# Kernel tuning notes

Hardware: AMD Instinct MI355X
Metric: run time of the kernel (lower is better)

The kernel has to match this reference:

```python
import jax, jax.numpy as jnp
import numpy as np

B, NWORD, HID = 4, 24, 512


def setup_inputs() -> dict:
    key = jax.random.key(0)
    ks = jax.random.split(key, 7)
    H = HID
    scale_in = 1.0 / np.sqrt(H)
    return {
        "seqt": jax.random.normal(ks[0], (B, NWORD, 2 * H), dtype=jnp.float32),
        # ins_input_linearity: Linear(H -> 5H) with bias
        "Wi": jax.random.normal(ks[1], (5 * H, H), dtype=jnp.float32) * scale_in,
        "bi": jnp.zeros((5 * H,), dtype=jnp.float32),
        # ins_state_linearity: Linear(H -> 5H) with bias (bias init: forget slots = 1)
        "Ws": jax.random.normal(ks[2], (5 * H, H), dtype=jnp.float32) * scale_in,
        "bs": jnp.zeros((5 * H,), dtype=jnp.float32).at[H:2 * H].set(1.0),
        # ins_bilinearity: BilinearSimilarity(2H, 2H) -> scalar x^T W y
        "Wbil": jax.random.normal(ks[3], (2 * H, 2 * H), dtype=jnp.float32) * (1.0 / (2.0 * H)),
    }


def reference(seqt, Wi, bi, Ws, bs, Wbil):
    """Inside pass (do_inside) of DioLstm in training mode (soft_sum over splits).

    Chart cell (left, L) covers words [left, left+L]. Returns root v = concat(h, c).
    """
    Bn, n, twoH = seqt.shape
    H = twoH // 2
    # ins_bias buffer: ones on the two forget-gate slots [H:3H]
    ins_bias = jnp.zeros((5 * H,), dtype=seqt.dtype).at[H:3 * H].set(1.0)

    def single(seq):  # seq: [n, 2H]
        chartH = jnp.zeros((n, n, H), seq.dtype).at[:, 0].set(seq[:, :H])
        chartC = jnp.zeros((n, n, H), seq.dtype).at[:, 0].set(seq[:, H:])
        chartS = jnp.zeros((n, n), seq.dtype)  # leaf scores are 0
        for L in range(1, n):  # span length - 1 (static unroll over diagonals)
            P = n - L  # number of spans on this diagonal
            lefts = jnp.arange(P)[:, None]          # [P,1]
            ksplit = jnp.arange(L)[None, :]          # [1,L]
            # left child: (left, k); right child: (left+k+1, L-1-k)
            lH = chartH[lefts, ksplit]; lC = chartC[lefts, ksplit]; lS = chartS[lefts, ksplit]
            ridx = lefts + ksplit + 1
            rlen = jnp.broadcast_to(L - 1 - ksplit, ridx.shape)
            rH = chartH[ridx, rlen]; rC = chartC[ridx, rlen]; rS = chartS[ridx, rlen]
            lv = jnp.concatenate([lH, lC], axis=-1)  # [P,L,2H]
            rv = jnp.concatenate([rH, rC], axis=-1)
            # bilinear compatibility + child scores
            compat = jnp.einsum('pki,ij,pkj->pk', lv, Wbil, rv) + lS + rS  # [P,L]
            # projected_input + projected_state (sum once; gate slices of the sum)
            proj = (lH @ Wi.T + bi + ins_bias) + (rH @ Ws.T + bs)  # [P,L,5H]
            ig, lf, rf, g, og = jnp.split(proj, 5, axis=-1)
            ig = jax.nn.sigmoid(ig); lf = jax.nn.sigmoid(lf); rf = jax.nn.sigmoid(rf)
            g = jnp.tanh(g); og = jax.nn.sigmoid(og)
            mem = lf * lC + rf * rC + ig * g
            h = og * jnp.tanh(mem)  # [P,L,H]
            # soft_sum: torch.tensor(s_set) detaches scores -> stop_gradient on weights
            sw = jax.lax.stop_gradient(compat)
            w = jax.nn.softmax(sw, axis=-1)  # [P,L]
            Hnew = jnp.einsum('pk,pkh->ph', w, h)
            Cnew = jnp.einsum('pk,pkh->ph', w, mem)
            Snew = jnp.sum(w * sw, axis=-1)
            pidx = jnp.arange(P)
            chartH = chartH.at[pidx, L].set(Hnew)
            chartC = chartC.at[pidx, L].set(Cnew)
            chartS = chartS.at[pidx, L].set(Snew)
        # root cell v = concat(h, c)
        return jnp.concatenate([chartH[0, n - 1], chartC[0, n - 1]], axis=0)

    return jax.vmap(single)(seqt)  # [B, 2H]
```

## Files before the change

### kernel.cpp

```cpp
#include <hip/hip_runtime.h>
#include <math.h>

#define NB 4
#define NW 24
#define H 512
#define H2 1024
#define H5 2560
#define NCELL 300
#define NEED_BYTES ((size_t)72<<20)

static float* g_buf = nullptr;
__attribute__((constructor)) static void dio_alloc_ws(){
  (void)hipMalloc((void**)&g_buf, NEED_BYTES);
}

typedef __attribute__((ext_vector_type(8))) short bf16x8;
typedef __attribute__((ext_vector_type(4))) float f32x4;
typedef unsigned short ushort_t;

__device__ __forceinline__ int coff(int l){ return l*NW - (l*(l-1))/2; }
__device__ __forceinline__ float sigm(float x){ return 1.f/(1.f+__expf(-x)); }
__device__ __forceinline__ float ftanh(float x){ return 1.f - 2.f/(__expf(2.f*x)+1.f); }

__device__ __forceinline__ ushort_t f2b(float x){
  unsigned int u = __float_as_uint(x);
  u += 0x7FFF + ((u>>16)&1);
  return (ushort_t)(u>>16);
}
__device__ __forceinline__ float b2f(ushort_t h){
  return __uint_as_float(((unsigned int)h)<<16);
}
__device__ __forceinline__ void split_store(ushort_t* __restrict__ ph,
                                            ushort_t* __restrict__ pl,
                                            size_t idx, float x){
  ushort_t h = f2b(x);
  ph[idx] = h;
  pl[idx] = f2b(x - b2f(h));
}

__device__ __forceinline__ float compat_dot(const float* __restrict__ cU,
                                            const float* __restrict__ cH,
                                            const float* __restrict__ cC,
                                            const float* __restrict__ cS,
                                            int lc, int rc, int lane){
  const float4* U4  = (const float4*)(cU + (size_t)lc*H2);
  const float4* Hr4 = (const float4*)(cH + (size_t)rc*H);
  const float4* Cr4 = (const float4*)(cC + (size_t)rc*H);
  float p = 0.f;
  #pragma unroll
  for (int it=0; it<2; it++){
    float4 u = U4[lane + 64*it], h = Hr4[lane + 64*it];
    p += u.x*h.x + u.y*h.y + u.z*h.z + u.w*h.w;
  }
  #pragma unroll
  for (int it=0; it<2; it++){
    float4 u = U4[128 + lane + 64*it], c = Cr4[lane + 64*it];
    p += u.x*c.x + u.y*c.y + u.z*c.z + u.w*c.w;
  }
  #pragma unroll
  for (int off=32; off>0; off>>=1) p += __shfl_down(p, off);
  return p + cS[lc] + cS[rc];
}

__global__ void k_init(const float* __restrict__ seqt,
                       const float* __restrict__ Wi, const float* __restrict__ Ws,
                       const float* __restrict__ Wbil,
                       ushort_t* __restrict__ WiBh, ushort_t* __restrict__ WiBl,
                       ushort_t* __restrict__ WsBh, ushort_t* __restrict__ WsBl,
                       ushort_t* __restrict__ WbilTh, ushort_t* __restrict__ WbilTl,
                       float* __restrict__ cH, float* __restrict__ cC, float* __restrict__ cS,
                       ushort_t* __restrict__ cHbh, ushort_t* __restrict__ cHbl,
                       ushort_t* __restrict__ cCbh, ushort_t* __restrict__ cCbl){
  const int blk = blockIdx.x, t = threadIdx.x;
  if (blk < 10240){
    int i = blk*256 + t;
    const int n = H5*H;
    if (i < n) split_store(WiBh, WiBl, i, Wi[i]);
    else       split_store(WsBh, WsBl, i-n, Ws[i-n]);
  } else if (blk < 11264){
    __shared__ float tile[32][33];
    int tb = blk - 10240;
    int tr = (tb>>5)*32, tc = (tb&31)*32;
    int tx = t & 31, ty = t >> 5;
    #pragma unroll
    for (int i=0;i<32;i+=8)
      tile[ty+i][tx] = Wbil[(size_t)(tr+ty+i)*H2 + tc+tx];
    __syncthreads();
    #pragma unroll
    for (int i=0;i<32;i+=8)
      split_store(WbilTh, WbilTl, (size_t)(tc+ty+i)*H2 + tr+tx, tile[tx][ty+i]);
  } else {
    int tid = (blk-11264)*256 + t;
    if (tid < NB*NW*H){
      int b = tid/(NW*H); int r = tid%(NW*H); int i = r/H; int d = r%H;
      size_t idx = (size_t)(b*NCELL + i)*H + d;
      float hv = seqt[(size_t)(b*NW+i)*H2 + d];
      float cv = seqt[(size_t)(b*NW+i)*H2 + H + d];
      cH[idx]=hv; cC[idx]=cv;
      split_store(cHbh,cHbl,idx,hv);
      split_store(cCbh,cCbl,idx,cv);
      if (d==0) cS[b*NCELL+i] = 0.f;
    }
  }
}

__device__ __forceinline__ void mfma3(f32x4& acc, bf16x8 ah, bf16x8 al,
                                      bf16x8 bh, bf16x8 bl){
  acc = __builtin_amdgcn_mfma_f32_16x16x32_bf16(ah, bh, acc, 0,0,0);
  acc = __builtin_amdgcn_mfma_f32_16x16x32_bf16(ah, bl, acc, 0,0,0);
  acc = __builtin_amdgcn_mfma_f32_16x16x32_bf16(al, bh, acc, 0,0,0);
}

__global__ void __launch_bounds__(512)
k_projN(const ushort_t* __restrict__ WiBh, const ushort_t* __restrict__ WiBl,
        const ushort_t* __restrict__ WsBh, const ushort_t* __restrict__ WsBl,
        const ushort_t* __restrict__ WbilTh, const ushort_t* __restrict__ WbilTl,
        const float* __restrict__ bi, const float* __restrict__ bs,
        const ushort_t* __restrict__ cHbh, const ushort_t* __restrict__ cHbl,
        const ushort_t* __restrict__ cCbh, const ushort_t* __restrict__ cCbl,
        float* __restrict__ cPI, float* __restrict__ cPS, float* __restrict__ cU,
        int d, int P)
{
  __shared__ f32x4 red[8][64];
  const int t = threadIdx.x, wave = t>>6, lane = t&63;
  const int jt = blockIdx.x;
  const int m0 = blockIdx.y*16;
  const int Mtot = NB*P;
  const int nm = min(16, Mtot-m0);

  int kind, j0;
  if (jt < 160){ kind=0; j0 = jt*16; }
  else if (jt < 320){ kind=1; j0 = (jt-160)*16; }
  else { kind=2; j0 = (jt-320)*16; }

  const int r = lane & 15;
  const int q = lane >> 4;

  int mg = m0 + (r < nm ? r : 0);
  const size_t arow = (size_t)((mg/P)*NCELL + coff(d) + mg%P)*H;

  f32x4 acc = {0.f,0.f,0.f,0.f};

  if (kind < 2){
    const ushort_t* bh_ = (kind==0 ? WiBh : WsBh) + (size_t)(j0+r)*H;
    const ushort_t* bl_ = (kind==0 ? WiBl : WsBl) + (size_t)(j0+r)*H;
    const int ks = wave*64 + q*8;
    bf16x8 fah[2], fal[2], fbh[2], fbl[2];
    #pragma unroll
    for (int s=0;s<2;s++){
      const int ko = ks + s*32;
      fah[s] = *(const bf16x8*)(cHbh + arow + ko);
      fal[s] = *(const bf16x8*)(cHbl + arow + ko);
      fbh[s] = *(const bf16x8*)(bh_ + ko);
      fbl[s] = *(const bf16x8*)(bl_ + ko);
    }
    #pragma unroll
    for (int s=0;s<2;s++) mfma3(acc, fah[s], fal[s], fbh[s], fbl[s]);
  } else {
    const ushort_t* bh_ = WbilTh + (size_t)(j0+r)*H2;
    const ushort_t* bl_ = WbilTl + (size_t)(j0+r)*H2;
    const ushort_t* ah_ = (wave<4 ? cHbh : cCbh) + arow;
    const ushort_t* al_ = (wave<4 ? cHbl : cCbl) + arow;
    const int kg0 = wave*128;
    const int ka0 = kg0 & 511;
    bf16x8 fah[4], fal[4], fbh[4], fbl[4];
    #pragma unroll
    for (int s=0;s<4;s++){
      const int so = s*32 + q*8;
      fah[s] = *(const bf16x8*)(ah_ + ka0 + so);
      fal[s] = *(const bf16x8*)(al_ + ka0 + so);
      fbh[s] = *(const bf16x8*)(bh_ + kg0 + so);
      fbl[s] = *(const bf16x8*)(bl_ + kg0 + so);
    }
    #pragma unroll
    for (int s=0;s<4;s++) mfma3(acc, fah[s], fal[s], fbh[s], fbl[s]);
  }

  red[wave][lane] = acc;
  __syncthreads();
  if (wave == 0){
    f32x4 s0=red[0][lane], s1=red[1][lane], s2=red[2][lane], s3=red[3][lane];
    f32x4 s4=red[4][lane], s5=red[5][lane], s6=red[6][lane], s7=red[7][lane];
    f32x4 tot = ((s0+s1)+(s2+s3)) + ((s4+s5)+(s6+s7));
    const int jo = j0 + r;
    float bias = 0.f;
    if (kind==0) bias = bi[jo] + ((jo>=H && jo<3*H)?1.f:0.f);
    else if (kind==1) bias = bs[jo];
    #pragma unroll
    for (int reg=0; reg<4; reg++){
      const int m = q*4 + reg;
      if (m < nm){
        const int mg2 = m0 + m;
        const size_t cell = (size_t)((mg2/P)*NCELL + coff(d) + mg2%P);
        const float v = tot[reg];
        if (kind==0)      cPI[cell*H5 + jo] = v + bias;
        else if (kind==1) cPS[cell*H5 + jo] = v + bias;
        else              cU [cell*H2 + jo] = v;
      }
    }
  }
}

__global__ void __launch_bounds__(256)
k_combine3(const float* __restrict__ cPI, const float* __restrict__ cPS,
           const float* __restrict__ cU,
           float* __restrict__ cH, float* __restrict__ cC, float* __restrict__ cS,
           ushort_t* __restrict__ cHbh, ushort_t* __restrict__ cHbl,
           ushort_t* __restrict__ cCbh, ushort_t* __restrict__ cCbl,
           const float* __restrict__ compatR, float* __restrict__ compatW,
           int L, int P){
  const int t = threadIdx.x;
  const int lane = t & 63;
  const int wave = t >> 6;
  const int nphase = NB*P*16;
  const int blk = blockIdx.x;

  if (blk >= nphase){
    const int P1 = P-1;
    const int nterm = L-1;
    int tid = (blk-nphase)*4 + wave;
    if (P1 > 0 && nterm > 0 && tid < NB*P1*nterm){
      int cell1 = tid / nterm;
      int k = 1 + tid % nterm;
      int b = cell1 / P1, left = cell1 % P1;
      int lc = b*NCELL + coff(k) + left;
      int rc = b*NCELL + coff(L-k) + left+k+1;
      float v = compat_dot(cU, cH, cC, cS, lc, rc, lane);
      if (lane==0) compatW[(b*NW + left)*NW + k] = v;
    }
    return;
  }

  const int cellid = blk >> 4;
  const int dg = blk & 15;
  const int b = cellid / P;
  const int left = cellid % P;
  __shared__ float compat_s[32];
  __shared__ float wts_s[32];
  __shared__ float S_s;
  __shared__ float partH[8][32];
  __shared__ float partC[8][32];

  if (wave == 0){
    int lc = b*NCELL + left;
    int rc = b*NCELL + coff(L-1) + left+1;
    float v = compat_dot(cU, cH, cC, cS, lc, rc, lane);
    if (lane==0) compat_s[0] = v;
  } else if (wave == 1 && L >= 2){
    int lc = b*NCELL + coff(L-1) + left;
    int rc = b*NCELL + left+L;
    float v = compat_dot(cU, cH, cC, cS, lc, rc, lane);
    if (lane==0) compat_s[L-1] = v;
  }
  if (t >= 1 && t <= L-2) compat_s[t] = compatR[(b*NW + left)*NW + t];
  __syncthreads();
  if (t==0){
    float mx = -1e30f;
    for (int k=0;k<L;k++) mx = fmaxf(mx, compat_s[k]);
    float den = 0.f;
    for (int k=0;k<L;k++){ float e = __expf(compat_s[k]-mx); wts_s[k]=e; den+=e; }
    float inv = 1.f/den, S = 0.f;
    for (int k=0;k<L;k++){ wts_s[k]*=inv; S += wts_s[k]*compat_s[k]; }
    S_s = S;
  }
  __syncthreads();
  const int dloc = t & 31;
  const int dim = dg*32 + dloc;
  const int kpar = t >> 5;
  float aH = 0.f, aC = 0.f;
  for (int k=kpar; k<L; k+=8){
    float wk = wts_s[k];
    int lc = b*NCELL + coff(k) + left;
    int rc = b*NCELL + coff(L-1-k) + left+k+1;
    const float* PI = cPI + (size_t)lc*H5;
    const float* PS = cPS + (size_t)rc*H5;
    float p0 = PI[dim]     + PS[dim];
    float p1 = PI[H+dim]   + PS[H+dim];
    float p2 = PI[2*H+dim] + PS[2*H+dim];
    float p3 = PI[3*H+dim] + PS[3*H+dim];
    float p4 = PI[4*H+dim] + PS[4*H+dim];
    float lcv = cC[(size_t)lc*H + dim];
    float rcv = cC[(size_t)rc*H + dim];
    float mem = sigm(p1)*lcv + sigm(p2)*rcv + sigm(p0)*ftanh(p3);
    float h = sigm(p4)*ftanh(mem);
    aH += wk*h; aC += wk*mem;
  }
  if (kpar > 0){ partH[kpar][dloc]=aH; partC[kpar][dloc]=aC; }
  __syncthreads();
  if (kpar == 0){
    #pragma unroll
    for (int q=1;q<8;q++){ aH += partH[q][dloc]; aC += partC[q][dloc]; }
    size_t nc = (size_t)(b*NCELL + coff(L) + left);
    cH[nc*H + dim] = aH;
    cC[nc*H + dim] = aC;
    split_store(cHbh,cHbl, nc*H + dim, aH);
    split_store(cCbh,cCbl, nc*H + dim, aC);
    if (t==0 && dg==0) cS[nc] = S_s;
  }
}

__global__ void k_out(const float* __restrict__ cH, const float* __restrict__ cC,
                      float* __restrict__ out){
  int tid = blockIdx.x*256+threadIdx.x;
  if (tid >= NB*H2) return;
  int b = tid>>10, d = tid&1023;
  int cell = b*NCELL + 299;
  out[tid] = (d<H) ? cH[(size_t)cell*H + d] : cC[(size_t)cell*H + (d-H)];
}

extern "C" void kernel_launch(void* const* d_in, const int* in_sizes, int n_in,
                              void* d_out, int out_size, void* d_ws, size_t ws_size,
                              hipStream_t stream){
  const float* seqt = (const float*)d_in[0];
  const float* Wi   = (const float*)d_in[1];
  const float* bi   = (const float*)d_in[2];
  const float* Ws   = (const float*)d_in[3];
  const float* bs   = (const float*)d_in[4];
  const float* Wbil = (const float*)d_in[5];
  float* out = (float*)d_out;

  float* p = (ws_size >= NEED_BYTES && g_buf == nullptr) ? (float*)d_ws : g_buf;
  float* cH  = p; p += (size_t)NB*NCELL*H;
  float* cC  = p; p += (size_t)NB*NCELL*H;
  float* cS  = p; p += (size_t)NB*NCELL;
  float* cPI = p; p += (size_t)NB*NCELL*H5;
  float* cPS = p; p += (size_t)NB*NCELL*H5;
  float* cU  = p; p += (size_t)NB*NCELL*H2;
  float* compatA = p; p += (size_t)NB*NW*NW;
  float* compatB = p; p += (size_t)NB*NW*NW;
  ushort_t* u = (ushort_t*)p;
  ushort_t* WiBh   = u; u += (size_t)H5*H;
  ushort_t* WiBl   = u; u += (size_t)H5*H;
  ushort_t* WsBh   = u; u += (size_t)H5*H;
  ushort_t* WsBl   = u; u += (size_t)H5*H;
  ushort_t* WbilTh = u; u += (size_t)H2*H2;
  ushort_t* WbilTl = u; u += (size_t)H2*H2;
  ushort_t* cHbh   = u; u += (size_t)NB*NCELL*H;
  ushort_t* cHbl   = u; u += (size_t)NB*NCELL*H;
  ushort_t* cCbh   = u; u += (size_t)NB*NCELL*H;
  ushort_t* cCbl   = u; u += (size_t)NB*NCELL*H;

  k_init<<<11456, 256, 0, stream>>>(seqt, Wi, Ws, Wbil,
      WiBh, WiBl, WsBh, WsBl, WbilTh, WbilTl,
      cH, cC, cS, cHbh, cHbl, cCbh, cCbl);

  k_projN<<<dim3(384, (NB*NW+15)/16), 512, 0, stream>>>(
      WiBh, WiBl, WsBh, WsBl, WbilTh, WbilTl, bi, bs,
      cHbh, cHbl, cCbh, cCbl, cPI, cPS, cU, 0, NW);
  for (int L=1; L<NW; L++){
    int P = NW - L;
    int P1 = P-1, nterm = L-1;
    int wblk = (P1>0 && nterm>0) ? (NB*P1*nterm + 3)/4 : 0;
    float* bufR = (L&1) ? compatA : compatB;
    float* bufW = (L&1) ? compatB : compatA;
    k_combine3<<<NB*P*16 + wblk, 256, 0, stream>>>(
        cPI, cPS, cU, cH, cC, cS, cHbh, cHbl, cCbh, cCbl,
        bufR, bufW, L, P);
    if (L < NW-1)
      k_projN<<<dim3(384, (NB*P+15)/16), 512, 0, stream>>>(
          WiBh, WiBl, WsBh, WsBl, WbilTh, WbilTl, bi, bs,
          cHbh, cHbl, cCbh, cCbl, cPI, cPS, cU, L, P);
  }
  k_out<<<16, 256, 0, stream>>>(cH, cC, out);
}
```

Baseline: 617.7 us.

## Replace per-diagonal kernel launches with a persistent work-stealing pipeline kernel

The roughly 47 launches of separate projection and combine kernels are replaced by one persistent kernel of 512 blocks. Blocks claim work through atomic counters and spin-wait on per-diagonal counters to enforce dependencies. The projection tile now loops over all rows of a batch per wave instead of reducing across waves in shared memory, and the final output is written directly, removing the k_out kernel. This is meant to remove launch gaps and barriers between diagonals, at the cost of spin-wait overhead, less parallelism per projection tile, and memory-ordering risk from relaxed atomics.

Measured after the change: 2.289 ms. +270.5%, slower.

```diff
diff --git a/kernel.cpp b/kernel.cpp
--- a/kernel.cpp
+++ b/kernel.cpp
@@ -8,6 +8,8 @@
 #define H5 2560
 #define NCELL 300
 #define NEED_BYTES ((size_t)72<<20)
+#define PGRID 512
+#define PTPB 256
 
 static float* g_buf = nullptr;
 __attribute__((constructor)) static void dio_alloc_ws(){
@@ -38,11 +40,27 @@
   pl[idx] = f2b(x - b2f(h));
 }
 
-__device__ __forceinline__ float compat_dot(const float* __restrict__ cU,
-                                            const float* __restrict__ cH,
-                                            const float* __restrict__ cC,
-                                            const float* __restrict__ cS,
-                                            int lc, int rc, int lane){
+__device__ __forceinline__ unsigned ldA(const unsigned* p){
+  return __hip_atomic_load(p, __ATOMIC_RELAXED, __HIP_MEMORY_SCOPE_AGENT);
+}
+__device__ __forceinline__ unsigned addA(unsigned* p, unsigned v){
+  return __hip_atomic_fetch_add(p, v, __ATOMIC_RELAXED, __HIP_MEMORY_SCOPE_AGENT);
+}
+__device__ __forceinline__ void stA(float* p, float v){
+  __hip_atomic_store((unsigned*)p, __float_as_uint(v),
+                     __ATOMIC_RELAXED, __HIP_MEMORY_SCOPE_AGENT);
+}
+__device__ __forceinline__ void stAu(unsigned* p, unsigned v){
+  __hip_atomic_store(p, v, __ATOMIC_RELAXED, __HIP_MEMORY_SCOPE_AGENT);
+}
+__device__ __forceinline__ void spin_ge(const unsigned* p, unsigned target){
+  while (ldA(p) < target) __builtin_amdgcn_s_sleep(8);
+}
+
+__device__ __forceinline__ float compat_dot2(const float* __restrict__ cU,
+                                             const float* __restrict__ cH,
+                                             const float* __restrict__ cC,
+                                             int lc, int rc, int lane){
   const float4* U4  = (const float4*)(cU + (size_t)lc*H2);
   const float4* Hr4 = (const float4*)(cH + (size_t)rc*H);
   const float4* Cr4 = (const float4*)(cC + (size_t)rc*H);
@@ -59,7 +77,7 @@
   }
   #pragma unroll
   for (int off=32; off>0; off>>=1) p += __shfl_down(p, off);
-  return p + cS[lc] + cS[rc];
+  return p;
 }
 
 __global__ void k_init(const float* __restrict__ seqt,
@@ -68,9 +86,11 @@
                        ushort_t* __restrict__ WiBh, ushort_t* __restrict__ WiBl,
                        ushort_t* __restrict__ WsBh, ushort_t* __restrict__ WsBl,
                        ushort_t* __restrict__ WbilTh, ushort_t* __restrict__ WbilTl,
-                       float* __restrict__ cH, float* __restrict__ cC, float* __restrict__ cS,
+                       float* __restrict__ cH, float* __restrict__ cC,
+                       float* __restrict__ cS2,
                        ushort_t* __restrict__ cHbh, ushort_t* __restrict__ cHbl,
-                       ushort_t* __restrict__ cCbh, ushort_t* __restrict__ cCbl){
+                       ushort_t* __restrict__ cCbh, ushort_t* __restrict__ cCbl,
+                       unsigned* __restrict__ ctr){
   const int blk = blockIdx.x, t = threadIdx.x;
   if (blk < 10240){
     int i = blk*256 + t;
@@ -89,7 +109,7 @@
     #pragma unroll
     for (int i=0;i<32;i+=8)
       split_store(WbilTh, WbilTl, (size_t)(tc+ty+i)*H2 + tr+tx, tile[tx][ty+i]);
-  } else {
+  } else if (blk < 11456){
     int tid = (blk-11264)*256 + t;
     if (tid < NB*NW*H){
       int b = tid/(NW*H); int r = tid%(NW*H); int i = r/H; int d = r%H;
@@ -99,8 +119,10 @@
       cH[idx]=hv; cC[idx]=cv;
       split_store(cHbh,cHbl,idx,hv);
       split_store(cCbh,cCbl,idx,cv);
-      if (d==0) cS[b*NCELL+i] = 0.f;
+      if (d==0) cS2[(b*NW + 0)*32 + i] = 0.f;
     }
+  } else {
+    for (int i=t; i<NW*192; i+=256) ctr[i] = 0u;
   }
 }
 
@@ -111,201 +133,257 @@
   acc = __builtin_amdgcn_mfma_f32_16x16x32_bf16(al, bh, acc, 0,0,0);
 }
 
-__global__ void __launch_bounds__(512)
-k_projN(const ushort_t* __restrict__ WiBh, const ushort_t* __restrict__ WiBl,
-        const ushort_t* __restrict__ WsBh, const ushort_t* __restrict__ WsBl,
-        const ushort_t* __restrict__ WbilTh, const ushort_t* __restrict__ WbilTl,
-        const float* __restrict__ bi, const float* __restrict__ bs,
-        const ushort_t* __restrict__ cHbh, const ushort_t* __restrict__ cHbl,
-        const ushort_t* __restrict__ cCbh, const ushort_t* __restrict__ cCbl,
-        float* __restrict__ cPI, float* __restrict__ cPS, float* __restrict__ cU,
-        int d, int P)
+__device__ __forceinline__ void proj_tile(
+    int b, int jt, int L, int Pd,
+    const ushort_t* __restrict__ WiBh, const ushort_t* __restrict__ WiBl,
+    const ushort_t* __restrict__ WsBh, const ushort_t* __restrict__ WsBl,
+    const ushort_t* __restrict__ WbilTh, const ushort_t* __restrict__ WbilTl,
+    const float* __restrict__ bi, const float* __restrict__ bs,
+    const ushort_t* __restrict__ cHbh, const ushort_t* __restrict__ cHbl,
+    const ushort_t* __restrict__ cCbh, const ushort_t* __restrict__ cCbl,
+    float* cPI, float* cPS, float* cU, int lane)
 {
-  __shared__ f32x4 red[8][64];
-  const int t = threadIdx.x, wave = t>>6, lane = t&63;
-  const int jt = blockIdx.x;
-  const int m0 = blockIdx.y*16;
-  const int Mtot = NB*P;
-  const int nm = min(16, Mtot-m0);
-
+  const int r = lane & 15, q = lane >> 4;
   int kind, j0;
   if (jt < 160){ kind=0; j0 = jt*16; }
   else if (jt < 320){ kind=1; j0 = (jt-160)*16; }
   else { kind=2; j0 = (jt-320)*16; }
-
-  const int r = lane & 15;
-  const int q = lane >> 4;
-
-  int mg = m0 + (r < nm ? r : 0);
-  const size_t arow = (size_t)((mg/P)*NCELL + coff(d) + mg%P)*H;
-
-  f32x4 acc = {0.f,0.f,0.f,0.f};
-
-  if (kind < 2){
-    const ushort_t* bh_ = (kind==0 ? WiBh : WsBh) + (size_t)(j0+r)*H;
-    const ushort_t* bl_ = (kind==0 ? WiBl : WsBl) + (size_t)(j0+r)*H;
-    const int ks = wave*64 + q*8;
-    bf16x8 fah[2], fal[2], fbh[2], fbl[2];
+  const int jo = j0 + r;
+  float bias = 0.f;
+  if (kind==0) bias = bi[jo] + ((jo>=H && jo<3*H)?1.f:0.f);
+  else if (kind==1) bias = bs[jo];
+  const f32x4 z4 = {0.f,0.f,0.f,0.f};
+
+  for (int m0 = 0; m0 < Pd; m0 += 16){
+    const int nm = (Pd - m0 < 16) ? (Pd - m0) : 16;
+    const int mg = m0 + (r < nm ? r : 0);
+    const size_t arow = (size_t)(b*NCELL + coff(L) + mg)*H;
+    f32x4 acc[8];
     #pragma unroll
-    for (int s=0;s<2;s++){
-      const int ko = ks + s*32;
-      fah[s] = *(const bf16x8*)(cHbh + arow + ko);
-      fal[s] = *(const bf16x8*)(cHbl + arow + ko);
-      fbh[s] = *(const bf16x8*)(bh_ + ko);
-      fbl[s] = *(const bf16x8*)(bl_ + ko);
+    for (int w=0;w<8;w++) acc[w] = z4;
+    if (kind < 2){
+      const ushort_t* bh_ = (kind==0 ? WiBh : WsBh) + (size_t)jo*H;
+      const ushort_t* bl_ = (kind==0 ? WiBl : WsBl) + (size_t)jo*H;
+      #pragma unroll
+      for (int w=0; w<8; w++){
+        #pragma unroll
+        for (int s=0;s<2;s++){
+          const int ko = w*64 + q*8 + s*32;
+          bf16x8 ah = *(const bf16x8*)(cHbh + arow + ko);
+          bf16x8 al = *(const bf16x8*)(cHbl + arow + ko);
+          bf16x8 bh = *(const bf16x8*)(bh_ + ko);
+          bf16x8 bl = *(const bf16x8*)(bl_ + ko);
+          mfma3(acc[w], ah, al, bh, bl);
+        }
+      }
+    } else {
+      const ushort_t* bh_ = WbilTh + (size_t)jo*H2;
+      const ushort_t* bl_ = WbilTl + (size_t)jo*H2;
+      #pragma unroll
+      for (int w=0; w<8; w++){
+        const ushort_t* ah_ = (w<4 ? cHbh : cCbh) + arow;
+        const ushort_t* al_ = (w<4 ? cHbl : cCbl) + arow;
+        const int kg0 = w*128, ka0 = kg0 & 511;
+        #pragma unroll
+        for (int s=0;s<4;s++){
+          const int so = s*32 + q*8;
+          bf16x8 ah = *(const bf16x8*)(ah_ + ka0 + so);
+          bf16x8 al = *(const bf16x8*)(al_ + ka0 + so);
+          bf16x8 bh = *(const bf16x8*)(bh_ + kg0 + so);
+          bf16x8 bl = *(const bf16x8*)(bl_ + kg0 + so);
+          mfma3(acc[w], ah, al, bh, bl);
+        }
+      }
     }
-    #pragma unroll
-    for (int s=0;s<2;s++) mfma3(acc, fah[s], fal[s], fbh[s], fbl[s]);
-  } else {
-    const ushort_t* bh_ = WbilTh + (size_t)(j0+r)*H2;
-    const ushort_t* bl_ = WbilTl + (size_t)(j0+r)*H2;
-    const ushort_t* ah_ = (wave<4 ? cHbh : cCbh) + arow;
-    const ushort_t* al_ = (wave<4 ? cHbl : cCbl) + arow;
-    const int kg0 = wave*128;
-    const int ka0 = kg0 & 511;
-    bf16x8 fah[4], fal[4], fbh[4], fbl[4];
-    #pragma unroll
-    for (int s=0;s<4;s++){
-      const int so = s*32 + q*8;
-      fah[s] = *(const bf16x8*)(ah_ + ka0 + so);
-      fal[s] = *(const bf16x8*)(al_ + ka0 + so);
-      fbh[s] = *(const bf16x8*)(bh_ + kg0 + so);
-      fbl[s] = *(const bf16x8*)(bl_ + kg0 + so);
-    }
-    #pragma unroll
-    for (int s=0;s<4;s++) mfma3(acc, fah[s], fal[s], fbh[s], fbl[s]);
-  }
-
-  red[wave][lane] = acc;
-  __syncthreads();
-  if (wave == 0){
-    f32x4 s0=red[0][lane], s1=red[1][lane], s2=red[2][lane], s3=red[3][lane];
-    f32x4 s4=red[4][lane], s5=red[5][lane], s6=red[6][lane], s7=red[7][lane];
-    f32x4 tot = ((s0+s1)+(s2+s3)) + ((s4+s5)+(s6+s7));
-    const int jo = j0 + r;
-    float bias = 0.f;
-    if (kind==0) bias = bi[jo] + ((jo>=H && jo<3*H)?1.f:0.f);
-    else if (kind==1) bias = bs[jo];
+    f32x4 tot = ((acc[0]+acc[1])+(acc[2]+acc[3])) + ((acc[4]+acc[5])+(acc[6]+acc[7]));
     #pragma unroll
     for (int reg=0; reg<4; reg++){
       const int m = q*4 + reg;
       if (m < nm){
-        const int mg2 = m0 + m;
-        const size_t cell = (size_t)((mg2/P)*NCELL + coff(d) + mg2%P);
+        const size_t cellj = (size_t)(b*NCELL + coff(L) + m0 + m);
         const float v = tot[reg];
-        if (kind==0)      cPI[cell*H5 + jo] = v + bias;
-        else if (kind==1) cPS[cell*H5 + jo] = v + bias;
-        else              cU [cell*H2 + jo] = v;
+        if (kind==0)      stA(&cPI[cellj*H5 + jo], v + bias);
+        else if (kind==1) stA(&cPS[cellj*H5 + jo], v + bias);
+        else              stA(&cU [cellj*H2 + jo], v);
       }
     }
   }
 }
 
-__global__ void __launch_bounds__(256)
-k_combine3(const float* __restrict__ cPI, const float* __restrict__ cPS,
-           const float* __restrict__ cU,
-           float* __restrict__ cH, float* __restrict__ cC, float* __restrict__ cS,
-           ushort_t* __restrict__ cHbh, ushort_t* __restrict__ cHbl,
-           ushort_t* __restrict__ cCbh, ushort_t* __restrict__ cCbl,
-           const float* __restrict__ compatR, float* __restrict__ compatW,
-           int L, int P){
-  const int t = threadIdx.x;
-  const int lane = t & 63;
-  const int wave = t >> 6;
-  const int nphase = NB*P*16;
-  const int blk = blockIdx.x;
-
-  if (blk >= nphase){
-    const int P1 = P-1;
-    const int nterm = L-1;
-    int tid = (blk-nphase)*4 + wave;
-    if (P1 > 0 && nterm > 0 && tid < NB*P1*nterm){
-      int cell1 = tid / nterm;
-      int k = 1 + tid % nterm;
-      int b = cell1 / P1, left = cell1 % P1;
-      int lc = b*NCELL + coff(k) + left;
-      int rc = b*NCELL + coff(L-k) + left+k+1;
-      float v = compat_dot(cU, cH, cC, cS, lc, rc, lane);
-      if (lane==0) compatW[(b*NW + left)*NW + k] = v;
-    }
-    return;
-  }
-
-  const int cellid = blk >> 4;
-  const int dg = blk & 15;
-  const int b = cellid / P;
-  const int left = cellid % P;
+__global__ void __launch_bounds__(PTPB)
+k_pipe(const ushort_t* __restrict__ WiBh, const ushort_t* __restrict__ WiBl,
+       const ushort_t* __restrict__ WsBh, const ushort_t* __restrict__ WsBl,
+       const ushort_t* __restrict__ WbilTh, const ushort_t* __restrict__ WbilTl,
+       const float* __restrict__ bi, const float* __restrict__ bs,
+       ushort_t* __restrict__ cHbh, ushort_t* __restrict__ cHbl,
+       ushort_t* __restrict__ cCbh, ushort_t* __restrict__ cCbl,
+       float* cPI, float* cPS, float* cU,
+       float* cH, float* cC, float* cS2, float* cmpT,
+       unsigned* ctr, float* __restrict__ out)
+{
   __shared__ float compat_s[32];
   __shared__ float wts_s[32];
   __shared__ float S_s;
   __shared__ float partH[8][32];
   __shared__ float partC[8][32];
-
-  if (wave == 0){
-    int lc = b*NCELL + left;
-    int rc = b*NCELL + coff(L-1) + left+1;
-    float v = compat_dot(cU, cH, cC, cS, lc, rc, lane);
-    if (lane==0) compat_s[0] = v;
-  } else if (wave == 1 && L >= 2){
-    int lc = b*NCELL + coff(L-1) + left;
-    int rc = b*NCELL + left+L;
-    float v = compat_dot(cU, cH, cC, cS, lc, rc, lane);
-    if (lane==0) compat_s[L-1] = v;
+  __shared__ int shi;
+
+  const int t = threadIdx.x, lane = t & 63, wave = t >> 6;
+
+  for (int L = 0; L < NW; L++){
+    const int Pd = NW - L;
+    unsigned* C = ctr + L*192;
+
+    if (L >= 1){
+      unsigned* Cp = ctr + (L-1)*192;
+      spin_ge(Cp + 96, (unsigned)(NB*96));
+      if (L >= 3) spin_ge(Cp + 160, (unsigned)(NB*Pd*(L-2)));
+
+      const int nA = NB*Pd*16;
+      for(;;){
+        __syncthreads();
+        if (t == 0){
+          unsigned cur = ldA(C + 0);
+          shi = (cur < (unsigned)nA) ? (int)addA(C + 0, 4u) : nA;
+        }
+        __syncthreads();
+        const int v0 = shi;
+        if (v0 >= nA) break;
+        const int ne = (nA - v0 < 4) ? (nA - v0) : 4;
+        for (int i = 0; i < ne; i++){
+          const int it = v0 + i;
+          const int dg = it & 15, cell = it >> 4;
+          const int b = cell / Pd, left = cell % Pd;
+          if (wave == 0){
+            int lc = b*NCELL + left;
+            int rc = b*NCELL + coff(L-1) + left+1;
+            float v = compat_dot2(cU, cH, cC, lc, rc, lane)
+                    + cS2[(b*NW + 0)*32 + left] + cS2[(b*NW + L-1)*32 + left+1];
+            if (lane==0) compat_s[0] = v;
+          } else if (wave == 1 && L >= 2){
+            int lc = b*NCELL + coff(L-1) + left;
+            int rc = b*NCELL + left+L;
+            float v = compat_dot2(cU, cH, cC, lc, rc, lane)
+                    + cS2[(b*NW + L-1)*32 + left] + cS2[(b*NW + 0)*32 + left+L];
+            if (lane==0) compat_s[L-1] = v;
+          }
+          if (t >= 1 && t <= L-2)
+            compat_s[t] = cmpT[((size_t)L*NB*NW + b*NW + left)*(size_t)NW + t];
+          __syncthreads();
+          if (t == 0){
+            float mx = -1e30f;
+            for (int k=0;k<L;k++) mx = fmaxf(mx, compat_s[k]);
+            float den = 0.f;
+            for (int k=0;k<L;k++){ float e = __expf(compat_s[k]-mx); wts_s[k]=e; den+=e; }
+            float inv = 1.f/den, S = 0.f;
+            for (int k=0;k<L;k++){ wts_s[k]*=inv; S += wts_s[k]*compat_s[k]; }
+            S_s = S;
+          }
+          __syncthreads();
+          const int dloc = t & 31;
+          const int dim = dg*32 + dloc;
+          const int kpar = t >> 5;
+          float aH = 0.f, aC = 0.f;
+          for (int k=kpar; k<L; k+=8){
+            float wk = wts_s[k];
+            int lc = b*NCELL + coff(k) + left;
+            int rc = b*NCELL + coff(L-1-k) + left+k+1;
+            const float* PI = cPI + (size_t)lc*H5;
+            const float* PS = cPS + (size_t)rc*H5;
+            float p0 = PI[dim]     + PS[dim];
+            float p1 = PI[H+dim]   + PS[H+dim];
+            float p2 = PI[2*H+dim] + PS[2*H+dim];
+            float p3 = PI[3*H+dim] + PS[3*H+dim];
+            float p4 = PI[4*H+dim] + PS[4*H+dim];
+            float lcv = cC[(size_t)lc*H + dim];
+            float rcv = cC[(size_t)rc*H + dim];
+            float mem = sigm(p1)*lcv + sigm(p2)*rcv + sigm(p0)*ftanh(p3);
+            float h = sigm(p4)*ftanh(mem);
+            aH += wk*h; aC += wk*mem;
+          }
+          if (kpar > 0){ partH[kpar][dloc]=aH; partC[kpar][dloc]=aC; }
+          __syncthreads();
+          if (kpar == 0){
+            #pragma unroll
+            for (int qq=1;qq<8;qq++){ aH += partH[qq][dloc]; aC += partC[qq][dloc]; }
+            if (L == NW-1){
+              out[b*H2 + dim]     = aH;
+              out[b*H2 + H + dim] = aC;
+            } else {
+              const size_t nc = (size_t)(b*NCELL + coff(L) + left);
+              stA(&cH[nc*H + dim], aH);
+              stA(&cC[nc*H + dim], aC);
+              ushort_t hH = f2b(aH), lH = f2b(aH - b2f(hH));
+              ushort_t hC = f2b(aC), lC = f2b(aC - b2f(hC));
+              unsigned nh = (unsigned)__shfl_down((int)hH, 1);
+              unsigned nl = (unsigned)__shfl_down((int)lH, 1);
+              unsigned mh = (unsigned)__shfl_down((int)hC, 1);
+              unsigned ml = (unsigned)__shfl_down((int)lC, 1);
+              if (!(t & 1)){
+                const size_t pi = (nc*H + dim) >> 1;
+                stAu((unsigned*)cHbh + pi, (unsigned)hH | (nh<<16));
+                stAu((unsigned*)cHbl + pi, (unsigned)lH | (nl<<16));
+                stAu((unsigned*)cCbh + pi, (unsigned)hC | (mh<<16));
+                stAu((unsigned*)cCbl + pi, (unsigned)lC | (ml<<16));
+              }
+              if (t == 0 && dg == 0) stA(&cS2[(b*NW + L)*32 + left], S_s);
+            }
+          }
+          __syncthreads();
+        }
+        __syncthreads();
+        if (t == 0) addA(C + 32, (unsigned)ne);
+      }
+
+      const int nWt = (L <= NW-2 && L >= 2) ? NB*(Pd-1)*(L-1) : 0;
+      if (nWt > 0) for(;;){
+        __syncthreads();
+        if (t == 0){
+          unsigned cur = ldA(C + 128);
+          shi = (cur < (unsigned)nWt) ? (int)addA(C + 128, 4u) : nWt;
+        }
+        __syncthreads();
+        const int w0 = shi;
+        if (w0 >= nWt) break;
+        const int w = w0 + wave;
+        if (w < nWt){
+          const int per = (Pd-1)*(L-1);
+          const int b = w / per, rr = w % per;
+          const int left = rr / (L-1);
+          const int k = 1 + rr % (L-1);
+          int lc = b*NCELL + coff(k) + left;
+          int rc = b*NCELL + coff(L-k) + left+k+1;
+          float v = compat_dot2(cU, cH, cC, lc, rc, lane)
+                  + cS2[(b*NW + k)*32 + left] + cS2[(b*NW + (L-k))*32 + left+k+1];
+          if (lane == 0)
+            stA(&cmpT[((size_t)(L+1)*NB*NW + b*NW + left)*(size_t)NW + k], v);
+        }
+        __syncthreads();
+        if (t == 0) addA(C + 160, (unsigned)((nWt - w0 < 4) ? (nWt - w0) : 4));
+      }
+
+      if (L == NW-1) break;
+      spin_ge(C + 32, (unsigned)(NB*Pd*16));
+    }
+
+    const int nB = NB*96;
+    for(;;){
+      __syncthreads();
+      if (t == 0){
+        unsigned cur = ldA(C + 64);
+        shi = (cur < (unsigned)nB) ? (int)addA(C + 64, 1u) : nB;
+      }
+      __syncthreads();
+      const int g = shi;
+      if (g >= nB) break;
+      const int b = g / 96, grp = g % 96;
+      proj_tile(b, grp*4 + wave, L, Pd,
+                WiBh, WiBl, WsBh, WsBl, WbilTh, WbilTl, bi, bs,
+                cHbh, cHbl, cCbh, cCbl, cPI, cPS, cU, lane);
+      __syncthreads();
+      if (t == 0) addA(C + 96, 1u);
+    }
   }
-  if (t >= 1 && t <= L-2) compat_s[t] = compatR[(b*NW + left)*NW + t];
-  __syncthreads();
-  if (t==0){
-    float mx = -1e30f;
-    for (int k=0;k<L;k++) mx = fmaxf(mx, compat_s[k]);
-    float den = 0.f;
-    for (int k=0;k<L;k++){ float e = __expf(compat_s[k]-mx); wts_s[k]=e; den+=e; }
-    float inv = 1.f/den, S = 0.f;
-    for (int k=0;k<L;k++){ wts_s[k]*=inv; S += wts_s[k]*compat_s[k]; }
-    S_s = S;
-  }
-  __syncthreads();
-  const int dloc = t & 31;
-  const int dim = dg*32 + dloc;
-  const int kpar = t >> 5;
-  float aH = 0.f, aC = 0.f;
-  for (int k=kpar; k<L; k+=8){
-    float wk = wts_s[k];
-    int lc = b*NCELL + coff(k) + left;
-    int rc = b*NCELL + coff(L-1-k) + left+k+1;
-    const float* PI = cPI + (size_t)lc*H5;
-    const float* PS = cPS + (size_t)rc*H5;
-    float p0 = PI[dim]     + PS[dim];
-    float p1 = PI[H+dim]   + PS[H+dim];
-    float p2 = PI[2*H+dim] + PS[2*H+dim];
-    float p3 = PI[3*H+dim] + PS[3*H+dim];
-    float p4 = PI[4*H+dim] + PS[4*H+dim];
-    float lcv = cC[(size_t)lc*H + dim];
-    float rcv = cC[(size_t)rc*H + dim];
-    float mem = sigm(p1)*lcv + sigm(p2)*rcv + sigm(p0)*ftanh(p3);
-    float h = sigm(p4)*ftanh(mem);
-    aH += wk*h; aC += wk*mem;
-  }
-  if (kpar > 0){ partH[kpar][dloc]=aH; partC[kpar][dloc]=aC; }
-  __syncthreads();
-  if (kpar == 0){
-    #pragma unroll
-    for (int q=1;q<8;q++){ aH += partH[q][dloc]; aC += partC[q][dloc]; }
-    size_t nc = (size_t)(b*NCELL + coff(L) + left);
-    cH[nc*H + dim] = aH;
-    cC[nc*H + dim] = aC;
-    split_store(cHbh,cHbl, nc*H + dim, aH);
-    split_store(cCbh,cCbl, nc*H + dim, aC);
-    if (t==0 && dg==0) cS[nc] = S_s;
-  }
-}
-
-__global__ void k_out(const float* __restrict__ cH, const float* __restrict__ cC,
-                      float* __restrict__ out){
-  int tid = blockIdx.x*256+threadIdx.x;
-  if (tid >= NB*H2) return;
-  int b = tid>>10, d = tid&1023;
-  int cell = b*NCELL + 299;
-  out[tid] = (d<H) ? cH[(size_t)cell*H + d] : cC[(size_t)cell*H + (d-H)];
 }
 
 extern "C" void kernel_launch(void* const* d_in, const int* in_sizes, int n_in,
@@ -320,14 +398,13 @@
   float* out = (float*)d_out;
 
   float* p = (ws_size >= NEED_BYTES && g_buf == nullptr) ? (float*)d_ws : g_buf;
-  float* cH  = p; p += (size_t)NB*NCELL*H;
-  float* cC  = p; p += (size_t)NB*NCELL*H;
-  float* cS  = p; p += (size_t)NB*NCELL;
-  float* cPI = p; p += (size_t)NB*NCELL*H5;
-  float* cPS = p; p += (size_t)NB*NCELL*H5;
-  float* cU  = p; p += (size_t)NB*NCELL*H2;
-  float* compatA = p; p += (size_t)NB*NW*NW;
-  float* compatB = p; p += (size_t)NB*NW*NW;
+  float* cH   = p; p += (size_t)NB*NCELL*H;
+  float* cC   = p; p += (size_t)NB*NCELL*H;
+  float* cPI  = p; p += (size_t)NB*NCELL*H5;
+  float* cPS  = p; p += (size_t)NB*NCELL*H5;
+  float* cU   = p; p += (size_t)NB*NCELL*H2;
+  float* cS2  = p; p += (size_t)NB*NW*32;
+  float* cmpT = p; p += (size_t)NW*NB*NW*NW;
   ushort_t* u = (ushort_t*)p;
   ushort_t* WiBh   = u; u += (size_t)H5*H;
   ushort_t* WiBl   = u; u += (size_t)H5*H;
@@ -339,27 +416,13 @@
   ushort_t* cHbl   = u; u += (size_t)NB*NCELL*H;
   ushort_t* cCbh   = u; u += (size_t)NB*NCELL*H;
   ushort_t* cCbl   = u; u += (size_t)NB*NCELL*H;
-
-  k_init<<<11456, 256, 0, stream>>>(seqt, Wi, Ws, Wbil,
+  unsigned* ctr    = (unsigned*)u;
+
+  k_init<<<11457, 256, 0, stream>>>(seqt, Wi, Ws, Wbil,
       WiBh, WiBl, WsBh, WsBl, WbilTh, WbilTl,
-      cH, cC, cS, cHbh, cHbl, cCbh, cCbl);
-
-  k_projN<<<dim3(384, (NB*NW+15)/16), 512, 0, stream>>>(
+      cH, cC, cS2, cHbh, cHbl, cCbh, cCbl, ctr);
+
+  k_pipe<<<PGRID, PTPB, 0, stream>>>(
       WiBh, WiBl, WsBh, WsBl, WbilTh, WbilTl, bi, bs,
-      cHbh, cHbl, cCbh, cCbl, cPI, cPS, cU, 0, NW);
-  for (int L=1; L<NW; L++){
-    int P = NW - L;
-    int P1 = P-1, nterm = L-1;
-    int wblk = (P1>0 && nterm>0) ? (NB*P1*nterm + 3)/4 : 0;
-    float* bufR = (L&1) ? compatA : compatB;
-    float* bufW = (L&1) ? compatB : compatA;
-    k_combine3<<<NB*P*16 + wblk, 256, 0, stream>>>(
-        cPI, cPS, cU, cH, cC, cS, cHbh, cHbl, cCbh, cCbl,
-        bufR, bufW, L, P);
-    if (L < NW-1)
-      k_projN<<<dim3(384, (NB*P+15)/16), 512, 0, stream>>>(
-          WiBh, WiBl, WsBh, WsBl, WbilTh, WbilTl, bi, bs,
-          cHbh, cHbl, cCbh, cCbl, cPI, cPS, cU, L, P);
-  }
-  k_out<<<16, 256, 0, stream>>>(cH, cC, out);
-}
+      cHbh, cHbl, cCbh, cCbl, cPI, cPS, cU, cH, cC, cS2, cmpT, ctr, out);
+}
```
